# Kernel optimization log

Hardware: AMD Instinct MI355X
Metric: run time of the kernel (lower is better)

Reference implementation:

```python
import jax, jax.numpy as jnp
import numpy as np

N, T, D, H, K = 2048, 128, 256, 256, 12
MAX_ITER = 100  # k-means max_iter from _cluster default


def setup_inputs() -> dict:
    key = jax.random.key(0)
    ks = jax.random.split(key, 16)
    std = 1.0 / np.sqrt(H).astype(np.float32)
    u = lambda k, shape: jax.random.uniform(k, shape, jnp.float32, -std, std)
    return {
        "x": jax.random.normal(ks[0], (N, T, D), jnp.float32),
        "lengths": jax.random.randint(ks[1], (N,), 1, T + 1),  # valid lens in [1, T]
        # GRU params (PyTorch layout: [3H, in], gate order r,z,n)
        "W_ih": u(ks[2], (3 * H, D)),
        "W_hh": u(ks[3], (3 * H, H)),
        "b_ih": u(ks[4], (3 * H,)),
        "b_hh": u(ks[5], (3 * H,)),
        # weight1 / weight2: nn.Linear(H, 1)
        "w1_w": u(ks[6], (1, H)), "w1_b": u(ks[7], (1,)),
        "w2_w": u(ks[8], (1, H)), "w2_b": u(ks[9], (1,)),
        # GCN layers: weight [H, H], bias [H]
        "g1_w": u(ks[10], (H, H)), "g1_b": u(ks[11], (H,)),
        "g2_w": u(ks[12], (H, H)), "g2_b": u(ks[13], (H,)),
    }


def _gru(x, W_ih, W_hh, b_ih, b_hh):
    # x: [N, T, D] -> outputs [T, N, H]
    def step(h, x_t):
        gx = x_t @ W_ih.T + b_ih          # [N, 3H]
        gh = h @ W_hh.T + b_hh            # [N, 3H]
        xr, xz, xn = jnp.split(gx, 3, axis=-1)
        hr, hz, hn = jnp.split(gh, 3, axis=-1)
        r = jax.nn.sigmoid(xr + hr)
        z = jax.nn.sigmoid(xz + hz)
        n = jnp.tanh(xn + r * hn)
        h_new = (1.0 - z) * n + z * h
        return h_new, h_new

    h0 = jnp.zeros((x.shape[0], W_hh.shape[1]), x.dtype)
    _, outs = jax.lax.scan(step, h0, jnp.swapaxes(x, 0, 1))
    return outs  # [T, N, H]


def _kmeans(data, k, max_iter=MAX_ITER):
    # data: [n, H]. Fixed-iteration Lloyd's: after convergence centers are a
    # fixed point, so running all max_iter iters matches the early-break loop.
    n = data.shape[0]
    idx = jax.random.permutation(jax.random.key(42), n)[:k]  # random init
    centers0 = data[idx]
    x2 = jnp.sum(data * data, axis=1, keepdims=True)  # [n, 1]

    def body(_, centers):
        # squared distances (same argmin as cdist)
        d2 = x2 - 2.0 * (data @ centers.T) + jnp.sum(centers * centers, axis=1)
        codes = jnp.argmin(d2, axis=1)  # [n]
        sums = jax.ops.segment_sum(data, codes, num_segments=k)       # [k, H]
        cnts = jax.ops.segment_sum(jnp.ones((n,), data.dtype), codes, num_segments=k)
        # empty clusters keep old center
        return jnp.where(cnts[:, None] > 0,
                         sums / jnp.maximum(cnts[:, None], 1.0),
                         centers)

    return jax.lax.fori_loop(0, max_iter, body, centers0)


def reference(x, lengths, W_ih, W_hh, b_ih, b_hh,
              w1_w, w1_b, w2_w, w2_b, g1_w, g1_b, g2_w, g2_b):
    outs = _gru(x, W_ih, W_hh, b_ih, b_hh)              # [T, N, H]
    n = x.shape[0]
    hidden_t = outs[lengths - 1, jnp.arange(n)]         # last valid step, [N, H]

    # clustering uses detached hidden states
    centers = _kmeans(jax.lax.stop_gradient(hidden_t), K)  # [K, H]

    e = jax.nn.relu(hidden_t @ centers.T)               # [N, K]
    scores = jax.nn.softmax(e, axis=-1)

    # adj = eye(K) so GraphConvolution reduces to an affine map
    h1 = jax.nn.relu(centers @ g1_w + g1_b)             # [K, H]
    h2 = jax.nn.relu(h1 @ g2_w + g2_b)                  # [K, H]

    clu_app = scores @ h2                               # [N, H]
    w1 = jax.nn.sigmoid(clu_app @ w1_w.T + w1_b)        # [N, 1]
    w2 = jax.nn.sigmoid(hidden_t @ w2_w.T + w2_b)       # [N, 1]
    w1n = w1 / (w1 + w2)
    return w1n * clu_app + (1.0 - w1n) * hidden_t       # [N, H]
```

## Files before the change

### kernel.cpp

```cpp
#include <hip/hip_runtime.h>
#include <hip/hip_cooperative_groups.h>
#include <cstdint>
#include <cstring>
#include <vector>
#include <algorithm>

namespace cg = cooperative_groups;


namespace {
constexpr int Nn = 2048;
constexpr int Tt = 128;
constexpr int Dd = 256;
constexpr int Hh = 256;
constexpr int Kk = 12;
constexpr int MAXIT = 100;
}

struct IdxArgs { int v[Kk]; };

typedef float v2f __attribute__((ext_vector_type(2)));

__device__ __forceinline__ float sigm(float x) { return 1.0f / (1.0f + expf(-x)); }

#if __has_builtin(__builtin_elementwise_fma)
#define PKFMA(A, X, W) (A) = __builtin_elementwise_fma((X), (W), (A))
#else
#define PKFMA(A, X, W) do { (A).x = __builtin_fmaf((X).x, (W).x, (A).x); \
                            (A).y = __builtin_fmaf((X).y, (W).y, (A).y); } while (0)
#endif
#define LO2(V) ((v2f){(V).x, (V).y})
#define HI2(V) ((v2f){(V).z, (V).w})

__global__ __launch_bounds__(64) void pack_w(
    const float* __restrict__ Wih, const float* __restrict__ Whh,
    float* __restrict__ pk)
{
  const int j = blockIdx.x;
  const int k4 = threadIdx.x;
  const int g = j >> 8, c = j & 255;
  float4 vih = *(const float4*)&Wih[(size_t)j * 256 + k4 * 4];
  float4 vhh = *(const float4*)&Whh[(size_t)j * 256 + k4 * 4];
  *(float4*)&pk[(((size_t)k4 * 6 + g) * 256 + c) * 4]       = vih;
  *(float4*)&pk[(((size_t)k4 * 6 + 3 + g) * 256 + c) * 4]   = vhh;
}

__global__ __launch_bounds__(512, 1) void gru_q(
    const float* __restrict__ x, const int* __restrict__ len,
    const float* __restrict__ pk,
    const float* __restrict__ bih, const float* __restrict__ bhh,
    float* __restrict__ hfin)
{
  __shared__ alignas(16) float xls[8][260];
  __shared__ alignas(16) float hls[8][260];
  __shared__ float4 pbuf[2][8][256];
  const int tid = threadIdx.x;
  const int cp = tid & 127;
  const int q  = tid >> 7;
  const int n0 = blockIdx.x * 8;
  const int C0 = cp, C1 = cp + 128;

  const float bir0 = bih[C0], bhr0 = bhh[C0];
  const float biz0 = bih[Hh + C0], bhz0 = bhh[Hh + C0];
  const float bin0 = bih[2 * Hh + C0], bhn0 = bhh[2 * Hh + C0];
  const float bir1 = bih[C1], bhr1 = bhh[C1];
  const float biz1 = bih[Hh + C1], bhz1 = bhh[Hh + C1];
  const float bin1 = bih[2 * Hh + C1], bhn1 = bhh[2 * Hh + C1];
  int L[8];
  #pragma unroll
  for (int r = 0; r < 8; ++r) L[r] = len[n0 + r];

  const int q16 = q * 16;
  const size_t cp4 = (size_t)cp * 4;

  if (tid < 256) {
    #pragma unroll
    for (int r = 0; r < 8; ++r) hls[r][tid] = 0.f;
  }

  for (int t = 0; t < Tt; ++t) {
    {
      int row = tid >> 6, c4 = tid & 63;
      *(float4*)&xls[row][c4 * 4] =
          *(const float4*)&x[(size_t)(n0 + row) * (Tt * Dd) + (size_t)t * Dd + c4 * 4];
    }
    __syncthreads();

    v2f aR[8][2] = {}, aZ[8][2] = {}, aXN[8][2] = {}, aHN[8][2] = {};

    #pragma unroll 1
    for (int i = 0; i < 16; ++i) {
      const int k4 = q16 + i;
      const float* pb = pk + (size_t)k4 * 6144 + cp4;
      float4 wr0 = *(const float4*)(pb);
      float4 wr1 = *(const float4*)(pb + 512);
      float4 wz0 = *(const float4*)(pb + 1024);
      float4 wz1 = *(const float4*)(pb + 1536);
      float4 wn0 = *(const float4*)(pb + 2048);
      float4 wn1 = *(const float4*)(pb + 2560);
      const int k = k4 * 4;
      #pragma unroll
      for (int r = 0; r < 8; ++r) {
        float4 xv = *(const float4*)&xls[r][k];
        v2f xlo = LO2(xv), xhi = HI2(xv);
        PKFMA(aR[r][0],  xlo, LO2(wr0)); PKFMA(aR[r][0],  xhi, HI2(wr0));
        PKFMA(aR[r][1],  xlo, LO2(wr1)); PKFMA(aR[r][1],  xhi, HI2(wr1));
        PKFMA(aZ[r][0],  xlo, LO2(wz0)); PKFMA(aZ[r][0],  xhi, HI2(wz0));
        PKFMA(aZ[r][1],  xlo, LO2(wz1)); PKFMA(aZ[r][1],  xhi, HI2(wz1));
        PKFMA(aXN[r][0], xlo, LO2(wn0)); PKFMA(aXN[r][0], xhi, HI2(wn0));
        PKFMA(aXN[r][1], xlo, LO2(wn1)); PKFMA(aXN[r][1], xhi, HI2(wn1));
      }
    }
    #pragma unroll 1
    for (int i = 0; i < 16; ++i) {
      const int k4 = q16 + i;
      const float* pb = pk + (size_t)k4 * 6144 + 3072 + cp4;
      float4 wr0 = *(const float4*)(pb);
      float4 wr1 = *(const float4*)(pb + 512);
      float4 wz0 = *(const float4*)(pb + 1024);
      float4 wz1 = *(const float4*)(pb + 1536);
      float4 wn0 = *(const float4*)(pb + 2048);
      float4 wn1 = *(const float4*)(pb + 2560);
      const int k = k4 * 4;
      #pragma unroll
      for (int r = 0; r < 8; ++r) {
        float4 hv = *(const float4*)&hls[r][k];
        v2f hlo = LO2(hv), hhi = HI2(hv);
        PKFMA(aR[r][0],  hlo, LO2(wr0)); PKFMA(aR[r][0],  hhi, HI2(wr0));
        PKFMA(aR[r][1],  hlo, LO2(wr1)); PKFMA(aR[r][1],  hhi, HI2(wr1));
        PKFMA(aZ[r][0],  hlo, LO2(wz0)); PKFMA(aZ[r][0],  hhi, HI2(wz0));
        PKFMA(aZ[r][1],  hlo, LO2(wz1)); PKFMA(aZ[r][1],  hhi, HI2(wz1));
        PKFMA(aHN[r][0], hlo, LO2(wn0)); PKFMA(aHN[r][0], hhi, HI2(wn0));
        PKFMA(aHN[r][1], hlo, LO2(wn1)); PKFMA(aHN[r][1], hhi, HI2(wn1));
      }
    }

    float fR[8][2], fZ[8][2], fX[8][2], fH[8][2];
    #pragma unroll
    for (int r = 0; r < 8; ++r) {
      fR[r][0] = aR[r][0].x + aR[r][0].y;  fR[r][1] = aR[r][1].x + aR[r][1].y;
      fZ[r][0] = aZ[r][0].x + aZ[r][0].y;  fZ[r][1] = aZ[r][1].x + aZ[r][1].y;
      fX[r][0] = aXN[r][0].x + aXN[r][0].y; fX[r][1] = aXN[r][1].x + aXN[r][1].y;
      fH[r][0] = aHN[r][0].x + aHN[r][0].y; fH[r][1] = aHN[r][1].x + aHN[r][1].y;
    }

    if (q == 1 || q == 3) {
      const int reg = q >> 1;
      #pragma unroll
      for (int r = 0; r < 8; ++r) {
        pbuf[reg][r][C0] = make_float4(fR[r][0], fZ[r][0], fX[r][0], fH[r][0]);
        pbuf[reg][r][C1] = make_float4(fR[r][1], fZ[r][1], fX[r][1], fH[r][1]);
      }
    }
    __syncthreads();
    if (q == 0 || q == 2) {
      const int reg = q >> 1;
      #pragma unroll
      for (int r = 0; r < 8; ++r) {
        float4 p0 = pbuf[reg][r][C0];
        float4 p1 = pbuf[reg][r][C1];
        fR[r][0] += p0.x; fZ[r][0] += p0.y; fX[r][0] += p0.z; fH[r][0] += p0.w;
        fR[r][1] += p1.x; fZ[r][1] += p1.y; fX[r][1] += p1.z; fH[r][1] += p1.w;
      }
    }
    __syncthreads();
    if (q == 2) {
      #pragma unroll
      for (int r = 0; r < 8; ++r) {
        pbuf[0][r][C0] = make_float4(fR[r][0], fZ[r][0], fX[r][0], fH[r][0]);
        pbuf[0][r][C1] = make_float4(fR[r][1], fZ[r][1], fX[r][1], fH[r][1]);
      }
    }
    __syncthreads();

    if (q == 0) {
      #pragma unroll
      for (int r = 0; r < 8; ++r) {
        if (t < L[r]) {
          float4 p0 = pbuf[0][r][C0];
          float4 p1 = pbuf[0][r][C1];
          float sR0 = fR[r][0] + p0.x, sZ0 = fZ[r][0] + p0.y;
          float sX0 = fX[r][0] + p0.z, sH0 = fH[r][0] + p0.w;
          float sR1 = fR[r][1] + p1.x, sZ1 = fZ[r][1] + p1.y;
          float sX1 = fX[r][1] + p1.z, sH1 = fH[r][1] + p1.w;
          float rg0 = sigm(sR0 + bir0 + bhr0);
          float zg0 = sigm(sZ0 + biz0 + bhz0);
          float ng0 = tanhf(sX0 + bin0 + rg0 * (sH0 + bhn0));
          float hv0 = (1.f - zg0) * ng0 + zg0 * hls[r][C0];
          float rg1 = sigm(sR1 + bir1 + bhr1);
          float zg1 = sigm(sZ1 + biz1 + bhz1);
          float ng1 = tanhf(sX1 + bin1 + rg1 * (sH1 + bhn1));
          float hv1 = (1.f - zg1) * ng1 + zg1 * hls[r][C1];
          hls[r][C0] = hv0;
          hls[r][C1] = hv1;
          if (t == L[r] - 1) {
            hfin[(size_t)(n0 + r) * Hh + C0] = hv0;
            hfin[(size_t)(n0 + r) * Hh + C1] = hv1;
          }
        }
      }
    }
  }
}

__global__ __launch_bounds__(256, 1) void km_coop(
    const float* __restrict__ hfin, float* __restrict__ cent,
    float* __restrict__ part, int* __restrict__ pcnt,
    int* __restrict__ gflag, IdxArgs ia)
{
  __shared__ alignas(16) float rows_l[32][260];
  __shared__ alignas(16) float cs[Kk][260];
  __shared__ float psl[Kk][256];
  __shared__ float c2s[Kk];
  __shared__ int codes_l[32];
  __shared__ int pcl[Kk];
  __shared__ int chg_l, brk_l;
  cg::grid_group grid = cg::this_grid();
  const int tid = threadIdx.x, lane = tid & 63, w = tid >> 6;
  const int blk = blockIdx.x, n0 = blk * 32;

  #pragma unroll
  for (int i = 0; i < 8; ++i) {
    int f = tid + i * 256;
    int row = f >> 6, c4 = f & 63;
    *(float4*)&rows_l[row][c4 * 4] =
        *(const float4*)&hfin[(size_t)(n0 + row) * Hh + c4 * 4];
  }
  if (tid < 32) codes_l[tid] = -1;
  if (blk == 0) {
    if (tid == 0) { gflag[0] = 0; gflag[1] = 0; }
    #pragma unroll
    for (int i = 0; i < 3; ++i) {
      int f = tid + i * 256;
      int k = f >> 6, c4 = f & 63;
      *(float4*)&cent[(size_t)k * Hh + c4 * 4] =
          *(const float4*)&hfin[(size_t)ia.v[k] * Hh + c4 * 4];
    }
  }
  __syncthreads();
  float4 v4[8];
  #pragma unroll
  for (int rr = 0; rr < 8; ++rr)
    v4[rr] = *(const float4*)&rows_l[w * 8 + rr][lane * 4];
  __threadfence();
  grid.sync();

  for (int it = 0; it < MAXIT; ++it) {
    #pragma unroll
    for (int i = 0; i < 3; ++i) {
      int f = tid + i * 256;
      int k = f >> 6, c4 = f & 63;
      float4 cv = (it == 0)
          ? *(const float4*)&hfin[(size_t)ia.v[k] * Hh + c4 * 4]
          : *(const float4*)&cent[(size_t)k * Hh + c4 * 4];
      *(float4*)&cs[k][c4 * 4] = cv;
    }
    if (tid == 0) chg_l = 0;
    if (tid < Kk) pcl[tid] = 0;
    __syncthreads();
    if (tid < Kk) {
      float s = 0.f;
      for (int c = 0; c < Hh; ++c) { float v = cs[tid][c]; s += v * v; }
      c2s[tid] = s;
    }
    __syncthreads();

    int mych = 0;
    #pragma unroll
    for (int rr = 0; rr < 8; ++rr) {
      const int row = w * 8 + rr;
      float best = 3.4e38f; int bi = 0;
      #pragma unroll
      for (int k = 0; k < Kk; ++k) {
        float4 cv = *(const float4*)&cs[k][lane * 4];
        float p = v4[rr].x * cv.x + v4[rr].y * cv.y
                + v4[rr].z * cv.z + v4[rr].w * cv.w;
        #pragma unroll
        for (int m = 1; m < 64; m <<= 1) p += __shfl_xor(p, m, 64);
        float d = c2s[k] - 2.f * p;
        if (d < best) { best = d; bi = k; }
      }
      if (lane == 0) {
        if (bi != codes_l[row]) mych = 1;
        codes_l[row] = bi;
      }
    }
    if (mych) atomicOr(&chg_l, 1);
    __syncthreads();

    #pragma unroll
    for (int k = 0; k < Kk; ++k) psl[k][tid] = 0.f;
    for (int r = 0; r < 32; ++r)
      psl[codes_l[r]][tid] += rows_l[r][tid];
    if (tid < 32) atomicAdd(&pcl[codes_l[tid]], 1);
    if (tid == 0 && chg_l) atomicOr(&gflag[it & 1], 1);
    __syncthreads();
    #pragma unroll
    for (int k = 0; k < Kk; ++k)
      part[((size_t)blk * Kk + k) * Hh + tid] = psl[k][tid];
    if (tid < Kk) pcnt[blk * Kk + tid] = pcl[tid];
    __threadfence();
    grid.sync();

    if (blk < Kk) {
      float s = 0.f;
      for (int p = 0; p < 64; ++p) s += part[((size_t)p * Kk + blk) * Hh + tid];
      int cn = 0;
      for (int p = 0; p < 64; ++p) cn += pcnt[p * Kk + blk];
      if (cn > 0) cent[(size_t)blk * Hh + tid] = s / (float)cn;
    }
    if (blk == 0 && tid == 0) gflag[(it + 1) & 1] = 0;
    __threadfence();
    grid.sync();
    if (tid == 0) brk_l = atomicAdd(&gflag[it & 1], 0);
    __syncthreads();
    if (brk_l == 0) break;
  }
}

__global__ __launch_bounds__(256) void gcn(
    const float* __restrict__ cent, const float* __restrict__ g1w,
    const float* __restrict__ g1b, const float* __restrict__ g2w,
    const float* __restrict__ g2b, float* __restrict__ h2out)
{
  __shared__ float a[Kk][Hh];
  __shared__ float b[Kk][Hh];
  int c = threadIdx.x;
  for (int i = c; i < Kk * Hh; i += 256) ((float*)a)[i] = cent[i];
  __syncthreads();
  float acc[Kk];
  #pragma unroll
  for (int k = 0; k < Kk; ++k) acc[k] = 0.f;
  for (int j = 0; j < Hh; ++j) {
    float wv = g1w[(size_t)j * Hh + c];
    #pragma unroll
    for (int k = 0; k < Kk; ++k) acc[k] += a[k][j] * wv;
  }
  #pragma unroll
  for (int k = 0; k < Kk; ++k) b[k][c] = fmaxf(acc[k] + g1b[c], 0.f);
  __syncthreads();
  #pragma unroll
  for (int k = 0; k < Kk; ++k) acc[k] = 0.f;
  for (int j = 0; j < Hh; ++j) {
    float wv = g2w[(size_t)j * Hh + c];
    #pragma unroll
    for (int k = 0; k < Kk; ++k) acc[k] += b[k][j] * wv;
  }
  #pragma unroll
  for (int k = 0; k < Kk; ++k) h2out[k * Hh + c] = fmaxf(acc[k] + g2b[c], 0.f);
}

__global__ __launch_bounds__(256) void finalk(
    const float* __restrict__ hfin, const float* __restrict__ cent,
    const float* __restrict__ h2, const float* __restrict__ w1w,
    const float* __restrict__ w1b, const float* __restrict__ w2w,
    const float* __restrict__ w2b, float* __restrict__ out)
{
  __shared__ alignas(16) float cs[Kk][Hh];
  __shared__ alignas(16) float hs[Kk][Hh];
  __shared__ float red[4];
  const int tid = threadIdx.x, lane = tid & 63, w = tid >> 6;
  const int n = blockIdx.x;
  for (int i = tid; i < Kk * Hh; i += 256) { ((float*)cs)[i] = cent[i]; ((float*)hs)[i] = h2[i]; }
  float ht = hfin[(size_t)n * Hh + tid];
  __syncthreads();

  auto bred = [&](float v) -> float {
    #pragma unroll
    for (int m = 1; m < 64; m <<= 1) v += __shfl_xor(v, m, 64);
    __syncthreads();
    if (lane == 0) red[w] = v;
    __syncthreads();
    return red[0] + red[1] + red[2] + red[3];
  };

  float ev[Kk];
  #pragma unroll
  for (int k = 0; k < Kk; ++k)
    ev[k] = fmaxf(bred(ht * cs[k][tid]), 0.f);

  float mx = ev[0];
  #pragma unroll
  for (int k = 1; k < Kk; ++k) mx = fmaxf(mx, ev[k]);
  float se = 0.f; float sc[Kk];
  #pragma unroll
  for (int k = 0; k < Kk; ++k) { sc[k] = expf(ev[k] - mx); se += sc[k]; }
  float inv = 1.f / se;
  float clu = 0.f;
  #pragma unroll
  for (int k = 0; k < Kk; ++k) clu += sc[k] * inv * hs[k][tid];

  float r1 = bred(clu * w1w[tid]);
  float r2 = bred(ht * w2w[tid]);
  float a1 = sigm(r1 + w1b[0]);
  float a2 = sigm(r2 + w2b[0]);
  float wn = a1 / (a1 + a2);
  out[(size_t)n * Hh + tid] = wn * clu + (1.f - wn) * ht;
}

static void tf2x32(uint32_t k0, uint32_t k1, uint32_t c0, uint32_t c1,
                   uint32_t& o0, uint32_t& o1) {
  uint32_t ks2 = k0 ^ k1 ^ 0x1BD11BDAu;
  uint32_t x0 = c0 + k0, x1 = c1 + k1;
#define TFR(r) do { x0 += x1; x1 = (x1 << (r)) | (x1 >> (32 - (r))); x1 ^= x0; } while (0)
  TFR(13); TFR(15); TFR(26); TFR(6);
  x0 += k1;  x1 += ks2 + 1u;
  TFR(17); TFR(29); TFR(16); TFR(24);
  x0 += ks2; x1 += k0 + 2u;
  TFR(13); TFR(15); TFR(26); TFR(6);
  x0 += k0;  x1 += k1 + 3u;
  TFR(17); TFR(29); TFR(16); TFR(24);
  x0 += k1;  x1 += ks2 + 4u;
  TFR(13); TFR(15); TFR(26); TFR(6);
  x0 += ks2; x1 += k0 + 5u;
#undef TFR
  o0 = x0; o1 = x1;
}

static void compute_idx(int* out12) {
  uint32_t kh = 0u, kl = 42u;
  std::vector<int> perm(Nn);
  for (int i = 0; i < Nn; ++i) perm[i] = i;
  std::vector<uint32_t> bits(Nn);
  std::vector<int> pos(Nn);
  for (int round = 0; round < 2; ++round) {
    uint32_t nh, nl, sh, sl;
    tf2x32(kh, kl, 0u, 0u, nh, nl);
    tf2x32(kh, kl, 0u, 1u, sh, sl);
    kh = nh; kl = nl;
    for (uint32_t i = 0; i < (uint32_t)Nn; ++i) {
      uint32_t o0, o1; tf2x32(sh, sl, 0u, i, o0, o1); bits[i] = o0 ^ o1;
    }
    for (int i = 0; i < Nn; ++i) pos[i] = i;
    std::stable_sort(pos.begin(), pos.end(),
                     [&](int a, int b) { return bits[a] < bits[b]; });
    std::vector<int> np(Nn);
    for (int i = 0; i < Nn; ++i) np[i] = perm[pos[i]];
    perm.swap(np);
  }
  for (int k = 0; k < Kk; ++k) out12[k] = perm[k];
}

extern "C" void kernel_launch(void* const* d_in, const int* in_sizes, int n_in,
                              void* d_out, int out_size, void* d_ws, size_t ws_size,
                              hipStream_t stream) {
  const float* x   = (const float*)d_in[0];
  const int*   len = (const int*)d_in[1];
  const float* Wih = (const float*)d_in[2];
  const float* Whh = (const float*)d_in[3];
  const float* bih = (const float*)d_in[4];
  const float* bhh = (const float*)d_in[5];
  const float* w1w = (const float*)d_in[6];
  const float* w1b = (const float*)d_in[7];
  const float* w2w = (const float*)d_in[8];
  const float* w2b = (const float*)d_in[9];
  const float* g1w = (const float*)d_in[10];
  const float* g1b = (const float*)d_in[11];
  const float* g2w = (const float*)d_in[12];
  const float* g2b = (const float*)d_in[13];
  float* out = (float*)d_out;

  float* wsf  = (float*)d_ws;
  float* hfin = wsf;
  float* cent = hfin + (size_t)Nn * Hh;
  float* h2g  = cent + Kk * Hh;
  float* part = h2g + Kk * Hh;
  int*   pcnt = (int*)(part + 64 * Kk * Hh);
  int*   gflag = pcnt + 768;
  float* pkw  = (float*)(pcnt + 1024);

  IdxArgs ia;
  compute_idx(ia.v);

  pack_w<<<768, 64, 0, stream>>>(Wih, Whh, pkw);
  gru_q<<<256, 512, 0, stream>>>(x, len, pkw, bih, bhh, hfin);

  {
    void* ka[] = {(void*)&hfin, (void*)&cent, (void*)&part, (void*)&pcnt,
                  (void*)&gflag, (void*)&ia};
    hipLaunchCooperativeKernel((const void*)km_coop, dim3(64), dim3(256),
                               ka, 0, stream);
  }

  gcn<<<1, 256, 0, stream>>>(cent, g1w, g1b, g2w, g2b, h2g);
  finalk<<<Nn, 256, 0, stream>>>(hfin, cent, h2g, w1w, w1b, w2w, w2b, out);
}
```

Baseline: 5.088 ms.

## Replicate centroid reduction per block to drop one grid sync per k-means iteration

Every block now reduces all partial sums and counts itself and keeps the centroids in shared memory. This removes the second grid-wide barrier and the global centroid round-trip in each iteration. Partial buffers are double-buffered by iteration parity, and the per-iteration change flags get their own slots to avoid races. In exchange, each block does 12x more redundant global reads for the reduction. Separately, the packed FMA macro is switched to inline v_pk_fma_f32 assembly in the GRU kernel.

```diff
diff --git a/kernel.cpp b/kernel.cpp
--- a/kernel.cpp
+++ b/kernel.cpp
@@ -23,12 +23,8 @@
 
 __device__ __forceinline__ float sigm(float x) { return 1.0f / (1.0f + expf(-x)); }
 
-#if __has_builtin(__builtin_elementwise_fma)
-#define PKFMA(A, X, W) (A) = __builtin_elementwise_fma((X), (W), (A))
-#else
-#define PKFMA(A, X, W) do { (A).x = __builtin_fmaf((X).x, (W).x, (A).x); \
-                            (A).y = __builtin_fmaf((X).y, (W).y, (A).y); } while (0)
-#endif
+#define PKFMA(A, X, W) \
+  asm("v_pk_fma_f32 %0, %1, %2, %0" : "+v"(A) : "v"(X), "v"(W))
 #define LO2(V) ((v2f){(V).x, (V).y})
 #define HI2(V) ((v2f){(V).z, (V).w})
 
@@ -214,6 +210,7 @@
   __shared__ float c2s[Kk];
   __shared__ int codes_l[32];
   __shared__ int pcl[Kk];
+  __shared__ int cnt_s[Kk];
   __shared__ int chg_l, brk_l;
   cg::grid_group grid = cg::this_grid();
   const int tid = threadIdx.x, lane = tid & 63, w = tid >> 6;
@@ -227,16 +224,14 @@
         *(const float4*)&hfin[(size_t)(n0 + row) * Hh + c4 * 4];
   }
   if (tid < 32) codes_l[tid] = -1;
-  if (blk == 0) {
-    if (tid == 0) { gflag[0] = 0; gflag[1] = 0; }
-    #pragma unroll
-    for (int i = 0; i < 3; ++i) {
-      int f = tid + i * 256;
-      int k = f >> 6, c4 = f & 63;
-      *(float4*)&cent[(size_t)k * Hh + c4 * 4] =
-          *(const float4*)&hfin[(size_t)ia.v[k] * Hh + c4 * 4];
-    }
-  }
+  #pragma unroll
+  for (int i = 0; i < 3; ++i) {
+    int f = tid + i * 256;
+    int k = f >> 6, c4 = f & 63;
+    *(float4*)&cs[k][c4 * 4] =
+        *(const float4*)&hfin[(size_t)ia.v[k] * Hh + c4 * 4];
+  }
+  if (blk == 0 && tid < MAXIT) gflag[tid] = 0;
   __syncthreads();
   float4 v4[8];
   #pragma unroll
@@ -246,15 +241,6 @@
   grid.sync();
 
   for (int it = 0; it < MAXIT; ++it) {
-    #pragma unroll
-    for (int i = 0; i < 3; ++i) {
-      int f = tid + i * 256;
-      int k = f >> 6, c4 = f & 63;
-      float4 cv = (it == 0)
-          ? *(const float4*)&hfin[(size_t)ia.v[k] * Hh + c4 * 4]
-          : *(const float4*)&cent[(size_t)k * Hh + c4 * 4];
-      *(float4*)&cs[k][c4 * 4] = cv;
-    }
     if (tid == 0) chg_l = 0;
     if (tid < Kk) pcl[tid] = 0;
     __syncthreads();
@@ -293,28 +279,46 @@
     for (int r = 0; r < 32; ++r)
       psl[codes_l[r]][tid] += rows_l[r][tid];
     if (tid < 32) atomicAdd(&pcl[codes_l[tid]], 1);
-    if (tid == 0 && chg_l) atomicOr(&gflag[it & 1], 1);
-    __syncthreads();
+    if (tid == 0 && chg_l) atomicOr(&gflag[it], 1);
+    __syncthreads();
+
+    float* pb = part + (size_t)(it & 1) * (64 * Kk * Hh);
+    int*   pc = pcnt + (it & 1) * (64 * Kk);
     #pragma unroll
     for (int k = 0; k < Kk; ++k)
-      part[((size_t)blk * Kk + k) * Hh + tid] = psl[k][tid];
-    if (tid < Kk) pcnt[blk * Kk + tid] = pcl[tid];
+      pb[((size_t)blk * Kk + k) * Hh + tid] = psl[k][tid];
+    if (tid < Kk) pc[blk * Kk + tid] = pcl[tid];
     __threadfence();
     grid.sync();
 
-    if (blk < Kk) {
+    if (tid == 0) brk_l = atomicAdd(&gflag[it], 0);
+    if (tid < Kk) {
+      int cn = 0;
+      for (int p = 0; p < 64; ++p) cn += pc[p * Kk + tid];
+      cnt_s[tid] = cn;
+    }
+    float sk[Kk];
+    #pragma unroll
+    for (int k = 0; k < Kk; ++k) {
       float s = 0.f;
-      for (int p = 0; p < 64; ++p) s += part[((size_t)p * Kk + blk) * Hh + tid];
-      int cn = 0;
-      for (int p = 0; p < 64; ++p) cn += pcnt[p * Kk + blk];
-      if (cn > 0) cent[(size_t)blk * Hh + tid] = s / (float)cn;
-    }
-    if (blk == 0 && tid == 0) gflag[(it + 1) & 1] = 0;
-    __threadfence();
-    grid.sync();
-    if (tid == 0) brk_l = atomicAdd(&gflag[it & 1], 0);
+      for (int p = 0; p < 64; ++p) s += pb[((size_t)p * Kk + k) * Hh + tid];
+      sk[k] = s;
+    }
+    __syncthreads();
+    #pragma unroll
+    for (int k = 0; k < Kk; ++k)
+      if (cnt_s[k] > 0) cs[k][tid] = sk[k] / (float)cnt_s[k];
     __syncthreads();
     if (brk_l == 0) break;
+  }
+
+  if (blk == 0) {
+    #pragma unroll
+    for (int i = 0; i < 3; ++i) {
+      int f = tid + i * 256;
+      int k = f >> 6, c4 = f & 63;
+      *(float4*)&cent[(size_t)k * Hh + c4 * 4] = *(const float4*)&cs[k][c4 * 4];
+    }
   }
 }
 
@@ -465,9 +469,9 @@
   float* cent = hfin + (size_t)Nn * Hh;
   float* h2g  = cent + Kk * Hh;
   float* part = h2g + Kk * Hh;
-  int*   pcnt = (int*)(part + 64 * Kk * Hh);
-  int*   gflag = pcnt + 768;
-  float* pkw  = (float*)(pcnt + 1024);
+  int*   pcnt = (int*)(part + 2 * 64 * Kk * Hh);
+  int*   gflag = pcnt + 2048;
+  float* pkw  = (float*)(gflag + 128);
 
   IdxArgs ia;
   compute_idx(ia.v);
```

New measurement: 5.863 ms. +15.2%, slower.
